# Performance work log

Hardware: AMD Instinct MI355X
Metric: run time of the kernel (lower is better)

## Reference

```python
import jax, jax.numpy as jnp
import numpy as np
from jax import lax

D_MODEL = 1024
LN_EPS = 1e-5


def setup_inputs() -> dict:
    key = jax.random.key(0)
    ks = jax.random.split(key, 9)
    B, L, D = 2, 2048, D_MODEL
    x = jax.random.normal(ks[0], (B, L, D), dtype=jnp.float32)
    A_param = jax.random.normal(ks[1], (D,), dtype=jnp.float32) * 0.1
    B_vec = jax.random.normal(ks[2], (D,), dtype=jnp.float32)
    C_vec = jax.random.normal(ks[3], (D,), dtype=jnp.float32)
    D_vec = jax.random.normal(ks[4], (D,), dtype=jnp.float32)
    # nn.Linear(d, d): weight (D, D) applied as x @ W.T + b
    W_proj = jax.random.normal(ks[5], (D, D), dtype=jnp.float32) * (1.0 / np.sqrt(D))
    b_proj = jax.random.normal(ks[6], (D,), dtype=jnp.float32) * 0.01
    gamma = jnp.ones((D,), dtype=jnp.float32)
    beta = jnp.zeros((D,), dtype=jnp.float32)
    return {"x": x, "A_param": A_param, "B_vec": B_vec, "C_vec": C_vec,
            "D_vec": D_vec, "W_proj": W_proj, "b_proj": b_proj,
            "gamma": gamma, "beta": beta}


def _layer_norm(x, gamma, beta):
    mu = jnp.mean(x, axis=-1, keepdims=True)
    var = jnp.mean(jnp.square(x - mu), axis=-1, keepdims=True)
    return (x - mu) * lax.rsqrt(var + LN_EPS) * gamma + beta


def reference(x, A_param, B_vec, C_vec, D_vec, W_proj, b_proj, gamma, beta):
    Bsz, L, D = x.shape
    A = jax.nn.sigmoid(A_param)                      # (D,)
    t = jnp.arange(L, dtype=jnp.float32)             # (L,)
    A_t = A[:, None] ** t[None, :]                   # (D, L) geometric decay
    K = (C_vec[:, None] * A_t * B_vec[:, None])[:, None, :]  # (D, 1, L)
    x_t = jnp.transpose(x, (0, 2, 1))                # (B, D, L)
    # depthwise cross-correlation with padding L-1 on both sides (matches torch F.conv1d)
    out = lax.conv_general_dilated(
        x_t, K, window_strides=(1,), padding=[(L - 1, L - 1)],
        dimension_numbers=("NCH", "OIH", "NCH"), feature_group_count=D)
    out = out[..., :L] + D_vec[None, :, None] * x_t  # (B, D, L)
    out = jnp.transpose(out, (0, 2, 1))              # (B, L, D)
    out = jnp.dot(jax.nn.gelu(out, approximate=False), W_proj.T) + b_proj
    return _layer_norm(x + out, gamma, beta)
```

## Files before the change

### kernel.cpp

```cpp
#include <hip/hip_runtime.h>
#include <hip/hip_bf16.h>
#include <math.h>

#define D_MODEL 1024
#define LSEQ 2048
#define BATCH 2
#define NROWS (BATCH*LSEQ)
#define NACT 16
#define CHSL 16

typedef __bf16 bf16;
typedef __attribute__((ext_vector_type(8))) __bf16 bf16x8;
typedef __attribute__((ext_vector_type(4))) __bf16 bf16x4;
typedef __attribute__((ext_vector_type(4))) float f32x4;

__device__ __forceinline__ float sigA(float ap) {
    return fmaxf(1.0f / (1.0f + expf(-ap)), 1e-30f);
}

__device__ __forceinline__ void gload_lds16(const void* g, void* l) {
    __builtin_amdgcn_global_load_lds(
        (const __attribute__((address_space(1))) void*)g,
        (__attribute__((address_space(3))) void*)l, 16, 0, 0);
}

__global__ __launch_bounds__(256) void k_misc(const float* __restrict__ W, bf16* __restrict__ Wb,
                                              const float* __restrict__ x,
                                              const float* __restrict__ A_param,
                                              float* __restrict__ partial) {
    if (blockIdx.x < 1024) {
        int idx = (blockIdx.x * 256 + threadIdx.x) * 4;
        f32x4 v = *reinterpret_cast<const f32x4*>(W + idx);
        bf16x4 o;
        #pragma unroll
        for (int k = 0; k < 4; ++k) o[k] = (bf16)v[k];
        *reinterpret_cast<bf16x4*>(Wb + idx) = o;
        return;
    }
    const int flat = blockIdx.x - 1024;
    const int c = flat & 15, dg = (flat >> 4) & 3, b = flat >> 6;
    const int d = dg * 256 + threadIdx.x;
    const float A = sigA(A_param[d]);
    const float l2A = log2f(A);
    const int s0 = c * CHSL;
    float w = exp2f((float)s0 * l2A);
    float sum = 0.0f;
    const int jmax = (c == NACT - 1) ? (LSEQ - s0) : CHSL;
    if (w != 0.0f) {
        const float* xp = x + ((size_t)b * LSEQ + s0) * D_MODEL + d;
        for (int j0 = 0; j0 < jmax; j0 += 8) {
            if (w == 0.0f) break;
            #pragma unroll
            for (int j = 0; j < 8; ++j) {
                sum += w * xp[(size_t)(j0 + j) * D_MODEL];
                w *= A;
            }
        }
    }
    partial[((size_t)b * NACT + c) * D_MODEL + d] = sum;
}

__global__ __launch_bounds__(256) void k_prep(const float* __restrict__ x,
                                              const float* __restrict__ A_param,
                                              const float* __restrict__ Bv,
                                              const float* __restrict__ Cv,
                                              const float* __restrict__ Dv,
                                              const float* __restrict__ partial,
                                              bf16* __restrict__ G) {
    const int ib = blockIdx.x, b = blockIdx.z;
    const int i0 = ib * 4;
    const int d0 = threadIdx.x * 4;
    f32x4 P = {0.f, 0.f, 0.f, 0.f};
    #pragma unroll
    for (int c = 0; c < NACT; ++c)
        P += *reinterpret_cast<const f32x4*>(partial + ((size_t)b * NACT + c) * D_MODEL + d0);
    float A4[4], coeff[4], dvv[4], w[4];
    #pragma unroll
    for (int k = 0; k < 4; ++k) {
        A4[k] = sigA(A_param[d0 + k]);
        float l2 = log2f(A4[k]);
        coeff[k] = Cv[d0 + k] * Bv[d0 + k] * P[k];
        dvv[k] = Dv[d0 + k];
        w[k] = exp2f((float)(LSEQ - 1 - (i0 + 3)) * l2);
    }
    #pragma unroll
    for (int j = 3; j >= 0; --j) {
        const int i = i0 + j;
        f32x4 xv = *reinterpret_cast<const f32x4*>(x + ((size_t)b * LSEQ + i) * D_MODEL + d0);
        bf16x4 g;
        #pragma unroll
        for (int k = 0; k < 4; ++k) {
            float u = coeff[k] * w[k] + dvv[k] * xv[k];
            g[k] = (bf16)(0.5f * u * (1.0f + erff(u * 0.70710678118654752f)));
            w[k] *= A4[k];
        }
        *reinterpret_cast<bf16x4*>(G + ((size_t)b * LSEQ + i) * D_MODEL + d0) = g;
    }
}

__global__ __launch_bounds__(256) void k_gemm(const bf16* __restrict__ G,
                                              const bf16* __restrict__ Wb,
                                              const float* __restrict__ bias,
                                              bf16* __restrict__ Z) {
    __shared__ __align__(16) bf16 S[3 * 12288];
    const int tid = threadIdx.x;
    const int lane = tid & 63, wave = tid >> 6;
    const int bid = blockIdx.x;
    const int bx = (bid & 7) * 8 + ((bid >> 3) & 7);
    const int by = bid >> 6;
    const int row0 = bx * 64, col0 = by * 128;
    const int wr = wave >> 1, wc = wave & 1;
    const int fr = lane & 15, q = lane >> 4;
    const int fx = fr & 7;
    f32x4 acc[2][4] = {};

    const int lr8 = lane >> 3;
    const int sb = 16 * ((lane & 7) ^ lr8);
    const bf16* srcbase[6];
    #pragma unroll
    for (int r = 0; r < 6; ++r) {
        const int c = wave * 6 + r;
        const bf16* mat;
        int row;
        if (c < 8) { mat = G;  row = row0 + c * 8 + lr8; }
        else       { mat = Wb; row = col0 + (c - 8) * 8 + lr8; }
        srcbase[r] = (const bf16*)((const char*)(mat + (size_t)row * D_MODEL) + sb);
    }

    auto stage = [&](int buf, int k0) {
        #pragma unroll
        for (int r = 0; r < 6; ++r)
            gload_lds16(srcbase[r] + k0, &S[buf * 12288 + (wave * 6 + r) * 512]);
    };

    bf16x8 aE[2][2], bE[4][2], aO[2][2], bO[4][2];

    auto readFrags = [&](int bufI, bf16x8 (&a)[2][2], bf16x8 (&bb)[4][2]) {
        const bf16* SA = &S[bufI * 12288];
        const bf16* SB = SA + 4096;
        #pragma unroll
        for (int fm = 0; fm < 2; ++fm)
            #pragma unroll
            for (int ks = 0; ks < 2; ++ks)
                a[fm][ks] = *reinterpret_cast<const bf16x8*>(
                    SA + (wr * 32 + fm * 16 + fr) * 64 + 8 * ((4 * ks + q) ^ fx));
        #pragma unroll
        for (int fn = 0; fn < 4; ++fn)
            #pragma unroll
            for (int ks = 0; ks < 2; ++ks)
                bb[fn][ks] = *reinterpret_cast<const bf16x8*>(
                    SB + (wc * 64 + fn * 16 + fr) * 64 + 8 * ((4 * ks + q) ^ fx));
    };

    auto mfmaAll = [&](bf16x8 (&a)[2][2], bf16x8 (&bb)[4][2]) {
        __builtin_amdgcn_s_setprio(1);
        #pragma unroll
        for (int fm = 0; fm < 2; ++fm)
            #pragma unroll
            for (int fn = 0; fn < 4; ++fn)
                #pragma unroll
                for (int ks = 0; ks < 2; ++ks)
                    acc[fm][fn] = __builtin_amdgcn_mfma_f32_16x16x32_bf16(a[fm][ks], bb[fn][ks], acc[fm][fn], 0, 0, 0);
        __builtin_amdgcn_s_setprio(0);
    };

    stage(0, 0);
    stage(1, 64);
    asm volatile("s_waitcnt vmcnt(6)" ::: "memory");
    __builtin_amdgcn_s_barrier();
    __builtin_amdgcn_sched_barrier(0);
    readFrags(0, aE, bE);

    #define ITER_BODY(T, ACUR, BCUR, ANXT, BNXT)                                   \
    {                                                                              \
        if ((T) + 2 < 16) stage(((T) + 2) % 3, ((T) + 2) * 64);                    \
        __builtin_amdgcn_sched_barrier(0);                                         \
        asm volatile("s_waitcnt lgkmcnt(0)" ::: "memory");                         \
        if ((T) + 2 < 16)      asm volatile("s_waitcnt vmcnt(6)" ::: "memory");    \
        else if ((T) + 1 < 16) asm volatile("s_waitcnt vmcnt(0)" ::: "memory");    \
        __builtin_amdgcn_sched_barrier(0);                                         \
        __builtin_amdgcn_s_barrier();                                              \
        __builtin_amdgcn_sched_barrier(0);                                         \
        if ((T) + 1 < 16) readFrags(((T) + 1) % 3, ANXT, BNXT);                    \
        mfmaAll(ACUR, BCUR);                                                       \
    }

    #pragma unroll
    for (int tt = 0; tt < 16; tt += 2) {
        ITER_BODY(tt, aE, bE, aO, bO);
        ITER_BODY(tt + 1, aO, bO, aE, bE);
    }
    #undef ITER_BODY

    #pragma unroll
    for (int fm = 0; fm < 2; ++fm) {
        const int rbase = row0 + wr * 32 + fm * 16 + (lane >> 4) * 4;
        #pragma unroll
        for (int fn = 0; fn < 4; ++fn) {
            const int c = col0 + wc * 64 + fn * 16 + fr;
            const float bv = bias[c];
            #pragma unroll
            for (int r = 0; r < 4; ++r)
                Z[(size_t)(rbase + r) * D_MODEL + c] = (bf16)(acc[fm][fn][r] + bv);
        }
    }
}

__global__ __launch_bounds__(256) void k_ln(const bf16* __restrict__ Z,
                                            const float* __restrict__ x,
                                            const float* __restrict__ gamma,
                                            const float* __restrict__ beta,
                                            float* __restrict__ out) {
    const int w = threadIdx.x >> 6, lane = threadIdx.x & 63;
    const int row = blockIdx.x * 4 + w;
    const bf16* zr = Z + (size_t)row * D_MODEL;
    const float* xr = x + (size_t)row * D_MODEL;
    float z[4][4];
    float s = 0.0f, sq = 0.0f;
    #pragma unroll
    for (int c = 0; c < 4; ++c) {
        const int d = c * 256 + lane * 4;
        bf16x4 zv = *reinterpret_cast<const bf16x4*>(zr + d);
        f32x4 xv = *reinterpret_cast<const f32x4*>(xr + d);
        #pragma unroll
        for (int k = 0; k < 4; ++k) {
            float v = xv[k] + (float)zv[k];
            z[c][k] = v; s += v; sq += v * v;
        }
    }
    #pragma unroll
    for (int o = 1; o < 64; o <<= 1) { s += __shfl_xor(s, o, 64); sq += __shfl_xor(sq, o, 64); }
    const float mu = s * (1.0f / D_MODEL);
    const float var = sq * (1.0f / D_MODEL) - mu * mu;
    const float inv = rsqrtf(var + 1e-5f);
    float* outr = out + (size_t)row * D_MODEL;
    #pragma unroll
    for (int c = 0; c < 4; ++c) {
        const int d = c * 256 + lane * 4;
        f32x4 g = *reinterpret_cast<const f32x4*>(gamma + d);
        f32x4 be = *reinterpret_cast<const f32x4*>(beta + d);
        f32x4 o;
        #pragma unroll
        for (int k = 0; k < 4; ++k) o[k] = (z[c][k] - mu) * inv * g[k] + be[k];
        *reinterpret_cast<f32x4*>(outr + d) = o;
    }
}

extern "C" void kernel_launch(void* const* d_in, const int* in_sizes, int n_in,
                              void* d_out, int out_size, void* d_ws, size_t ws_size,
                              hipStream_t stream) {
    const float* x       = (const float*)d_in[0];
    const float* A_param = (const float*)d_in[1];
    const float* B_vec   = (const float*)d_in[2];
    const float* C_vec   = (const float*)d_in[3];
    const float* D_vec   = (const float*)d_in[4];
    const float* W       = (const float*)d_in[5];
    const float* b_proj  = (const float*)d_in[6];
    const float* gamma   = (const float*)d_in[7];
    const float* beta    = (const float*)d_in[8];
    float* out = (float*)d_out;

    char* ws = (char*)d_ws;
    float* partial = (float*)ws;
    bf16*  Wb      = (bf16*)(ws + (128 << 10));
    bf16*  G       = (bf16*)(ws + (128 << 10) + (2 << 20));
    bf16*  Z       = (bf16*)(ws + (128 << 10) + (10 << 20));

    hipLaunchKernelGGL(k_misc, dim3(1152), dim3(256), 0, stream, W, Wb, x, A_param, partial);
    hipLaunchKernelGGL(k_prep, dim3(LSEQ / 4, 1, BATCH), dim3(256), 0, stream,
                       x, A_param, B_vec, C_vec, D_vec, partial, G);
    hipLaunchKernelGGL(k_gemm, dim3(512), dim3(256), 0, stream, G, Wb, b_proj, Z);
    hipLaunchKernelGGL(k_ln,   dim3(NROWS / 4), dim3(256), 0, stream, Z, x, gamma, beta, out);
}
```

Baseline: 41.35 us.

## Move W conversion into prep kernel, swizzle row mapping, vectorize GEMM stores

The W fp32-to-bf16 conversion moves out of the decay kernel into extra blocks of the prep kernel, so the short decay-sum kernel runs alone and the conversion overlaps with G construction. The prep and LayerNorm kernels remap block indices so consecutive blocks are spread across row ranges, likely to spread rows across XCDs or L2 slices. The GEMM swaps the MFMA operands so each lane holds four consecutive columns, which allows packed bf16x4 stores and vector bias loads instead of scattered scalar stores. The risks are a longer critical path in prep and the correctness of the transposed accumulator layout.

```diff
diff --git a/kernel.cpp b/kernel.cpp
--- a/kernel.cpp
+++ b/kernel.cpp
@@ -24,21 +24,11 @@
         (__attribute__((address_space(3))) void*)l, 16, 0, 0);
 }
 
-__global__ __launch_bounds__(256) void k_misc(const float* __restrict__ W, bf16* __restrict__ Wb,
-                                              const float* __restrict__ x,
-                                              const float* __restrict__ A_param,
-                                              float* __restrict__ partial) {
-    if (blockIdx.x < 1024) {
-        int idx = (blockIdx.x * 256 + threadIdx.x) * 4;
-        f32x4 v = *reinterpret_cast<const f32x4*>(W + idx);
-        bf16x4 o;
-        #pragma unroll
-        for (int k = 0; k < 4; ++k) o[k] = (bf16)v[k];
-        *reinterpret_cast<bf16x4*>(Wb + idx) = o;
-        return;
-    }
-    const int flat = blockIdx.x - 1024;
-    const int c = flat & 15, dg = (flat >> 4) & 3, b = flat >> 6;
+__global__ __launch_bounds__(256) void k_decay(const float* __restrict__ x,
+                                               const float* __restrict__ A_param,
+                                               float* __restrict__ partial) {
+    const int bid = blockIdx.x;
+    const int c = bid & 15, dg = (bid >> 4) & 3, b = bid >> 6;
     const int d = dg * 256 + threadIdx.x;
     const float A = sigA(A_param[d]);
     const float l2A = log2f(A);
@@ -66,10 +56,28 @@
                                               const float* __restrict__ Cv,
                                               const float* __restrict__ Dv,
                                               const float* __restrict__ partial,
+                                              const float* __restrict__ W,
+                                              bf16* __restrict__ Wb,
                                               bf16* __restrict__ G) {
-    const int ib = blockIdx.x, b = blockIdx.z;
-    const int i0 = ib * 4;
-    const int d0 = threadIdx.x * 4;
+    const int bid = blockIdx.x;
+    const int tid = threadIdx.x;
+    if (bid >= 1024) {
+        const int base = bid - 1024;
+        #pragma unroll
+        for (int it = 0; it < 4; ++it) {
+            const int idx = ((base * 256 + tid) + it * 65536) * 4;
+            f32x4 v = *reinterpret_cast<const f32x4*>(W + idx);
+            bf16x4 o;
+            #pragma unroll
+            for (int k = 0; k < 4; ++k) o[k] = (bf16)v[k];
+            *reinterpret_cast<bf16x4*>(Wb + idx) = o;
+        }
+        return;
+    }
+    const int r0 = (bid & 7) * 512 + (bid >> 3) * 4;
+    const int b = r0 >> 11;
+    const int i0 = r0 & 2047;
+    const int d0 = tid * 4;
     f32x4 P = {0.f, 0.f, 0.f, 0.f};
     #pragma unroll
     for (int c = 0; c < NACT; ++c)
@@ -160,7 +168,7 @@
             for (int fn = 0; fn < 4; ++fn)
                 #pragma unroll
                 for (int ks = 0; ks < 2; ++ks)
-                    acc[fm][fn] = __builtin_amdgcn_mfma_f32_16x16x32_bf16(a[fm][ks], bb[fn][ks], acc[fm][fn], 0, 0, 0);
+                    acc[fm][fn] = __builtin_amdgcn_mfma_f32_16x16x32_bf16(bb[fn][ks], a[fm][ks], acc[fm][fn], 0, 0, 0);
         __builtin_amdgcn_s_setprio(0);
     };
 
@@ -194,14 +202,15 @@
 
     #pragma unroll
     for (int fm = 0; fm < 2; ++fm) {
-        const int rbase = row0 + wr * 32 + fm * 16 + (lane >> 4) * 4;
+        const int row = row0 + wr * 32 + fm * 16 + fr;
         #pragma unroll
         for (int fn = 0; fn < 4; ++fn) {
-            const int c = col0 + wc * 64 + fn * 16 + fr;
-            const float bv = bias[c];
-            #pragma unroll
-            for (int r = 0; r < 4; ++r)
-                Z[(size_t)(rbase + r) * D_MODEL + c] = (bf16)(acc[fm][fn][r] + bv);
+            const int c0 = col0 + wc * 64 + fn * 16 + q * 4;
+            f32x4 bv = *reinterpret_cast<const f32x4*>(bias + c0);
+            bf16x4 pk;
+            #pragma unroll
+            for (int r = 0; r < 4; ++r) pk[r] = (bf16)(acc[fm][fn][r] + bv[r]);
+            *reinterpret_cast<bf16x4*>(&Z[(size_t)row * D_MODEL + c0]) = pk;
         }
     }
 }
@@ -212,7 +221,7 @@
                                             const float* __restrict__ beta,
                                             float* __restrict__ out) {
     const int w = threadIdx.x >> 6, lane = threadIdx.x & 63;
-    const int row = blockIdx.x * 4 + w;
+    const int row = (blockIdx.x & 7) * 512 + (blockIdx.x >> 3) * 4 + w;
     const bf16* zr = Z + (size_t)row * D_MODEL;
     const float* xr = x + (size_t)row * D_MODEL;
     float z[4][4];
@@ -266,9 +275,9 @@
     bf16*  G       = (bf16*)(ws + (128 << 10) + (2 << 20));
     bf16*  Z       = (bf16*)(ws + (128 << 10) + (10 << 20));
 
-    hipLaunchKernelGGL(k_misc, dim3(1152), dim3(256), 0, stream, W, Wb, x, A_param, partial);
-    hipLaunchKernelGGL(k_prep, dim3(LSEQ / 4, 1, BATCH), dim3(256), 0, stream,
-                       x, A_param, B_vec, C_vec, D_vec, partial, G);
-    hipLaunchKernelGGL(k_gemm, dim3(512), dim3(256), 0, stream, G, Wb, b_proj, Z);
-    hipLaunchKernelGGL(k_ln,   dim3(NROWS / 4), dim3(256), 0, stream, Z, x, gamma, beta, out);
-}
+    hipLaunchKernelGGL(k_decay, dim3(128), dim3(256), 0, stream, x, A_param, partial);
+    hipLaunchKernelGGL(k_prep,  dim3(1280), dim3(256), 0, stream,
+                       x, A_param, B_vec, C_vec, D_vec, partial, W, Wb, G);
+    hipLaunchKernelGGL(k_gemm,  dim3(512), dim3(256), 0, stream, G, Wb, b_proj, Z);
+    hipLaunchKernelGGL(k_ln,    dim3(1024), dim3(256), 0, stream, Z, x, gamma, beta, out);
+}
```

Result: no change. 41.68 us (+0.8%).
